# Optimization experiments

Hardware: AMD Instinct MI355X
Metric: run time of the kernel (lower is better)

The kernel has to match this reference:

```python
import jax, jax.numpy as jnp
import numpy as np

NUM_USERS = 100000
NUM_ITEMS = 50000
N_NODES = NUM_USERS + NUM_ITEMS
D = 64                 # embed_dim (= user/item/cate embed dims)
NNZ = 2400000          # sparse adjacency nnz (avg degree 16)
B = 4096               # batch size
HIST = 50              # item history length (max)
UHIST = 30             # user history length (max)
MC = 5                 # max categories per item
NC = 1000              # num_cates
CONCAT = 3 * D         # 192 = user/item concat dim
INNER = 2 * CONCAT     # 384 = MLP expansion factor 2
NUM_GNN_LAYERS = 3


def setup_inputs() -> dict:
    ks = jax.random.split(jax.random.key(0), 20)
    emb_table = jax.random.normal(ks[0], (N_NODES, D), jnp.float32) * 0.02
    cate_table = jax.random.normal(ks[1], (NC, D), jnp.float32) * 0.02
    adj_rows = jax.random.randint(ks[2], (NNZ,), 0, N_NODES, jnp.int32)
    adj_cols = jax.random.randint(ks[3], (NNZ,), 0, N_NODES, jnp.int32)
    adj_vals = jax.random.uniform(ks[4], (NNZ,), jnp.float32) * (1.0 / 16.0)
    cates = jax.random.randint(ks[5], (NUM_ITEMS, MC), 0, NC, jnp.int32)
    cate_lens = jax.random.randint(ks[6], (NUM_ITEMS,), 1, MC + 1, jnp.int32)
    users = jax.random.randint(ks[7], (B,), 0, NUM_USERS, jnp.int32)
    items = jax.random.randint(ks[8], (B,), 0, NUM_ITEMS, jnp.int32)
    item_history_matrix = jax.random.randint(ks[9], (B, HIST), 0, NUM_ITEMS, jnp.int32)
    item_history_len = jax.random.randint(ks[10], (B,), 1, HIST + 1, jnp.int32)
    user_history_matrix = jax.random.randint(ks[11], (B, UHIST), 0, NUM_USERS, jnp.int32)
    user_history_len = jax.random.randint(ks[12], (B,), 1, UHIST + 1, jnp.int32)
    # 4 PreNormResidual MLP blocks: [user_mlp, user_mlp_2, item_mlp, item_mlp_2]
    mlp_ln_w = jnp.ones((4, CONCAT), jnp.float32)
    mlp_ln_b = jnp.zeros((4, CONCAT), jnp.float32)
    mlp_w1 = jax.random.normal(ks[13], (4, CONCAT, INNER), jnp.float32) * 0.05
    mlp_b1 = jnp.zeros((4, INNER), jnp.float32)
    mlp_w2 = jax.random.normal(ks[14], (4, INNER, CONCAT), jnp.float32) * 0.05
    mlp_b2 = jnp.zeros((4, CONCAT), jnp.float32)
    return dict(emb_table=emb_table, cate_table=cate_table, adj_vals=adj_vals,
                mlp_ln_w=mlp_ln_w, mlp_ln_b=mlp_ln_b, mlp_w1=mlp_w1, mlp_b1=mlp_b1,
                mlp_w2=mlp_w2, mlp_b2=mlp_b2, adj_rows=adj_rows, adj_cols=adj_cols,
                cates=cates, cate_lens=cate_lens, users=users, items=items,
                item_history_matrix=item_history_matrix, item_history_len=item_history_len,
                user_history_matrix=user_history_matrix, user_history_len=user_history_len)


def _avg_pool(emb, lens):
    # emb: [..., L, D], lens: [...] -> masked mean over L (matches average_pooling)
    L = emb.shape[-2]
    mask = (jnp.arange(L) < lens[..., None]).astype(emb.dtype)[..., None]
    s = jnp.sum(emb * mask, axis=-2)
    c = jnp.sum(mask, axis=-2) + 1e-9
    return s / c


def _layernorm(x, w, b, eps=1e-5):
    mu = jnp.mean(x, axis=-1, keepdims=True)
    var = jnp.mean(jnp.square(x - mu), axis=-1, keepdims=True)
    return (x - mu) * jax.lax.rsqrt(var + eps) * w + b


def _forward(emb_table, cate_table, adj_vals, mlp_ln_w, mlp_ln_b, mlp_w1, mlp_b1,
             mlp_w2, mlp_b2, adj_rows, adj_cols, cates, cate_lens, users, items,
             item_history_matrix, item_history_len, user_history_matrix, user_history_len):
    n = emb_table.shape[0]
    # GNN propagation: mean of [e0, e1, e2, e3], e_{k+1} = A @ e_k (SpMM via segment_sum)
    e = emb_table
    acc = emb_table
    for _ in range(NUM_GNN_LAYERS):
        msgs = adj_vals[:, None] * e[adj_cols]          # [nnz, D]
        e = jax.ops.segment_sum(msgs, adj_rows, num_segments=n)
        acc = acc + e
    gnn = acc / float(NUM_GNN_LAYERS + 1)
    # --- user features ---
    static_u = gnn[users]                               # [B, D]
    hist_item = emb_table[item_history_matrix + NUM_USERS]   # [B, H, D]
    hc = cates[item_history_matrix]                     # [B, H, MC]
    hcl = cate_lens[item_history_matrix]                # [B, H]
    hce = cate_table[hc]                                # [B, H, MC, D]
    avg_cate = _avg_pool(hce, hcl)                      # [B, H, D]
    hist_with_cate = jnp.concatenate([hist_item, avg_cate], axis=-1)  # [B, H, 2D]
    user_hist = _avg_pool(hist_with_cate, item_history_len)           # [B, 2D]
    uf = jnp.concatenate([static_u, user_hist], axis=-1)              # [B, 3D]
    # --- item features ---
    static_i = gnn[items + NUM_USERS]                   # [B, D]
    ice = cate_table[cates[items]]                      # [B, MC, D]
    avg_ic = _avg_pool(ice, cate_lens[items])           # [B, D]
    item_with_cate = jnp.concatenate([static_i, avg_ic], axis=-1)     # [B, 2D]
    hu = emb_table[user_history_matrix]                 # [B, Hu, D]
    item_hist = _avg_pool(hu, user_history_len)         # [B, D]
    itf = jnp.concatenate([item_with_cate, item_hist], axis=-1)       # [B, 3D]
    # --- PreNormResidual MLP blocks ---
    def block(x, i):
        y = _layernorm(x, mlp_ln_w[i], mlp_ln_b[i])
        h = jax.nn.relu(y @ mlp_w1[i] + mlp_b1[i])
        return h @ mlp_w2[i] + mlp_b2[i] + x
    ue = block(uf, 0) + block(uf, 1)
    ie = block(itf, 2) + block(itf, 3)
    ue = ue / jnp.maximum(jnp.linalg.norm(ue, axis=-1, keepdims=True), 1e-12)
    ie = ie / jnp.maximum(jnp.linalg.norm(ie, axis=-1, keepdims=True), 1e-12)
    return ue, ie


def reference(emb_table, cate_table, adj_vals, mlp_ln_w, mlp_ln_b, mlp_w1, mlp_b1,
              mlp_w2, mlp_b2, adj_rows, adj_cols, cates, cate_lens, users, items,
              item_history_matrix, item_history_len, user_history_matrix, user_history_len):
    return _forward(emb_table, cate_table, adj_vals, mlp_ln_w, mlp_ln_b, mlp_w1, mlp_b1,
                    mlp_w2, mlp_b2, adj_rows, adj_cols, cates, cate_lens, users, items,
                    item_history_matrix, item_history_len, user_history_matrix, user_history_len)
```

## Files before the change

kernel.cpp:

```cpp
#include <hip/hip_runtime.h>
#include <hip/hip_bf16.h>
#include <cstdint>
#include <cstddef>

#define NU      100000
#define NN      150000
#define DDIM    64
#define NNZ_C   2400000
#define B_C     4096
#define HIST_C  50
#define UHIST_C 30
#define MC_C    5
#define CDIM    192
#define IDIM    384

#define NBUK    1176
#define BCAP    2560
#define SCAP    44
#define EPB     8192
#define EDGEH   293
#define FEAT_BLKS 2048
#define CONV_BLKS2 144
#define EMBC_BLKS 1172
#define SPMM_BLKS 4704
#define MARK_BLKS 1408

#define OFF_E1BF   0
#define OFF_E2BF   4816896
#define OFF_EMBBF  9633792
#define OFF_BKT    14433792
#define OFF_GCNT   20454912
#define OFF_SFB    20456192
#define OFF_FLAG   20460928
#define OFF_SDEG   20611456
#define OFF_SEDG   20619648
#define OFF_SIDX   21340544
#define OFF_ROWOFF 21491072
#define OFF_RDEG   21641600
#define OFF_UF     21792128
#define OFF_ITF    22578560
#define OFF_W1T    23364992
#define OFF_W2T    23512448
#define OFF_YBF    14433792
#define OFF_HBF    16006656
#define OFF_ZU     0
#define OFF_ZI     786432

typedef __bf16 bf16x8 __attribute__((ext_vector_type(8)));
typedef __bf16 bf16x4 __attribute__((ext_vector_type(4)));
typedef float f32x4 __attribute__((ext_vector_type(4)));

__device__ inline float4 ldb(const __bf16* p) {
  bf16x4 v = *(const bf16x4*)p;
  return make_float4((float)v[0], (float)v[1], (float)v[2], (float)v[3]);
}
__device__ inline void stb(__bf16* p, float4 o) {
  bf16x4 v;
  v[0] = (__bf16)o.x; v[1] = (__bf16)o.y; v[2] = (__bf16)o.z; v[3] = (__bf16)o.w;
  *(bf16x4*)p = v;
}

__device__ inline void xr4(float4& a) {
  a.x += __shfl_xor(a.x, 16, 64); a.y += __shfl_xor(a.y, 16, 64);
  a.z += __shfl_xor(a.z, 16, 64); a.w += __shfl_xor(a.w, 16, 64);
  a.x += __shfl_xor(a.x, 32, 64); a.y += __shfl_xor(a.y, 32, 64);
  a.z += __shfl_xor(a.z, 32, 64); a.w += __shfl_xor(a.w, 32, 64);
}

__global__ __launch_bounds__(256) void seedflag_kernel(
    const int* __restrict__ users, const int* __restrict__ items,
    int* __restrict__ sfb, int* __restrict__ sidx, int* __restrict__ flag) {
  int t = blockIdx.x * 256 + threadIdx.x;
  if (t >= 2 * B_C) return;
  int s = (t < B_C) ? users[t] : items[t - B_C] + NU;
  atomicOr(&sfb[s >> 5], (int)(1u << (s & 31)));
  sidx[s] = t;
  flag[s] = 1;
}

__global__ __launch_bounds__(256) void mega_kernel(
    const int* __restrict__ rows, const int* __restrict__ cols,
    const float* __restrict__ vals, const int* __restrict__ sfb,
    const int* __restrict__ sidx, int* __restrict__ sdeg,
    int2* __restrict__ sedg, int* __restrict__ gcnt, int2* __restrict__ bkt,
    const float* __restrict__ emb, const float* __restrict__ cate_table,
    const int* __restrict__ cates, const int* __restrict__ cate_lens,
    const int* __restrict__ items, const int* __restrict__ ihm,
    const int* __restrict__ ihl, const int* __restrict__ uhm,
    const int* __restrict__ uhl, float* __restrict__ uf,
    float* __restrict__ itf,
    const float* __restrict__ w1, const float* __restrict__ w2,
    __bf16* __restrict__ w1t, __bf16* __restrict__ w2t,
    __bf16* __restrict__ embbf) {
  __shared__ float tlds[64 * 65];
  __shared__ int hist[NBUK];
  __shared__ int cur[NBUK];
  int blk = blockIdx.x;
  if (blk < EDGEH) {
    int t = threadIdx.x;
    for (int i = t; i < NBUK; i += 256) hist[i] = 0;
    __syncthreads();
    int base = blk * EPB;
    for (int k = 0; k < EPB / 256; ++k) {
      int e = base + k * 256 + t;
      if (e < NNZ_C) atomicAdd(&hist[rows[e] >> 7], 1);
    }
    __syncthreads();
    for (int i = t; i < NBUK; i += 256) {
      int h = hist[i];
      cur[i] = h ? atomicAdd(&gcnt[i], h) : 0;
    }
    __syncthreads();
    for (int k = 0; k < EPB / 256; ++k) {
      int e = base + k * 256 + t;
      if (e < NNZ_C) {
        int r = rows[e], c = cols[e];
        float v = vals[e];
        int bk2 = r >> 7;
        int slot = atomicAdd(&cur[bk2], 1);
        if (slot < BCAP)
          bkt[(size_t)bk2 * BCAP + slot] = make_int2(((r & 127) << 18) | c, __float_as_int(v));
        if ((sfb[r >> 5] >> (r & 31)) & 1) {
          int si = sidx[r];
          int p = atomicAdd(&sdeg[si], 1);
          if (p < SCAP) sedg[(size_t)si * SCAP + p] = make_int2(c, __float_as_int(v));
        }
      }
    }
  } else if (blk < EDGEH + FEAT_BLKS) {
    int tid = threadIdx.x;
    int wave = tid >> 6, w = tid & 63, g = w >> 4, li = w & 15;
    int q = (blk - EDGEH) * 4 + wave;
    if (q < B_C) {
      int b = q;
      int len = ihl[b];
      float4 su = {0.f, 0.f, 0.f, 0.f}, sc = {0.f, 0.f, 0.f, 0.f};
      for (int h = g; h < len; h += 4) {
        int it = ihm[b * HIST_C + h];
        const float4 iv = *(const float4*)(emb + ((size_t)NU + it) * DDIM + li * 4);
        su.x += iv.x; su.y += iv.y; su.z += iv.z; su.w += iv.w;
        int cl = cate_lens[it];
        int id[5];
#pragma unroll
        for (int c = 0; c < 5; ++c) id[c] = cates[it * MC_C + c];
        float4 cs = {0.f, 0.f, 0.f, 0.f};
#pragma unroll
        for (int c = 0; c < 5; ++c) {
          if (c < cl) {
            const float4 cv = *(const float4*)(cate_table + (size_t)id[c] * DDIM + li * 4);
            cs.x += cv.x; cs.y += cv.y; cs.z += cv.z; cs.w += cv.w;
          }
        }
        float icl = 1.f / (float)cl;
        sc.x += cs.x * icl; sc.y += cs.y * icl; sc.z += cs.z * icl; sc.w += cs.w * icl;
      }
      xr4(su); xr4(sc);
      float inv = 1.f / (float)len;
      float* urow = uf + (size_t)b * CDIM;
      if (g == 0) {
        float4 o = {su.x * inv, su.y * inv, su.z * inv, su.w * inv};
        *(float4*)(urow + 64 + li * 4) = o;
      } else if (g == 1) {
        float4 o = {sc.x * inv, sc.y * inv, sc.z * inv, sc.w * inv};
        *(float4*)(urow + 128 + li * 4) = o;
      }
    } else {
      int b = q - B_C;
      int it = items[b];
      int cl = cate_lens[it];
      float4 cs = {0.f, 0.f, 0.f, 0.f};
      for (int c = g; c < cl; c += 4) {
        const float4 cv = *(const float4*)(cate_table + (size_t)cates[it * MC_C + c] * DDIM + li * 4);
        cs.x += cv.x; cs.y += cv.y; cs.z += cv.z; cs.w += cv.w;
      }
      int ul = uhl[b];
      float4 hs = {0.f, 0.f, 0.f, 0.f};
      for (int h = g; h < ul; h += 4) {
        const float4 hv = *(const float4*)(emb + (size_t)uhm[b * UHIST_C + h] * DDIM + li * 4);
        hs.x += hv.x; hs.y += hv.y; hs.z += hv.z; hs.w += hv.w;
      }
      xr4(cs); xr4(hs);
      float* irow = itf + (size_t)b * CDIM;
      if (g == 0) {
        float icl = 1.f / (float)cl;
        float4 o = {cs.x * icl, cs.y * icl, cs.z * icl, cs.w * icl};
        *(float4*)(irow + 64 + li * 4) = o;
      } else if (g == 1) {
        float iul = 1.f / (float)ul;
        float4 o = {hs.x * iul, hs.y * iul, hs.z * iul, hs.w * iul};
        *(float4*)(irow + 128 + li * 4) = o;
      }
    }
  } else if (blk < EDGEH + FEAT_BLKS + CONV_BLKS2) {
    int tile = blk - EDGEH - FEAT_BLKS;
    int t = threadIdx.x;
    if (tile < 72) {
      int p = tile / 18, r = tile % 18, kt = r / 6, nt = r % 6;
      int k0 = kt * 64, n0 = nt * 64;
      const float* srcp = w1 + (size_t)p * (CDIM * IDIM);
#pragma unroll
      for (int i = 0; i < 16; ++i) {
        int idx = i * 256 + t;
        int kl = idx >> 6, nl = idx & 63;
        tlds[kl * 65 + nl] = srcp[(size_t)(k0 + kl) * IDIM + n0 + nl];
      }
      __syncthreads();
#pragma unroll
      for (int i = 0; i < 16; ++i) {
        int idx = i * 256 + t;
        int nl = idx >> 6, kl = idx & 63;
        w1t[((size_t)p * IDIM + n0 + nl) * CDIM + k0 + kl] = (__bf16)tlds[kl * 65 + nl];
      }
    } else {
      int t2 = tile - 72;
      int p = t2 / 18, r = t2 % 18, kt = r / 3, nt = r % 3;
      int k0 = kt * 64, n0 = nt * 64;
      const float* srcp = w2 + (size_t)p * (IDIM * CDIM);
#pragma unroll
      for (int i = 0; i < 16; ++i) {
        int idx = i * 256 + t;
        int kl = idx >> 6, nl = idx & 63;
        tlds[kl * 65 + nl] = srcp[(size_t)(k0 + kl) * CDIM + n0 + nl];
      }
      __syncthreads();
#pragma unroll
      for (int i = 0; i < 16; ++i) {
        int idx = i * 256 + t;
        int nl = idx >> 6, kl = idx & 63;
        w2t[((size_t)p * CDIM + n0 + nl) * IDIM + k0 + kl] = (__bf16)tlds[kl * 65 + nl];
      }
    }
  } else {
    int base = (blk - EDGEH - FEAT_BLKS - CONV_BLKS2) * 2048 + threadIdx.x;
#pragma unroll
    for (int k = 0; k < 8; ++k) {
      int gidx = base + k * 256;
      if (gidx < 2400000) {
        float4 v = ((const float4*)emb)[gidx];
        stb(embbf + (size_t)gidx * 4, v);
      }
    }
  }
}

__global__ __launch_bounds__(256) void bucket_sort(
    int2* bkt, const int* __restrict__ gcnt,
    int* __restrict__ rowoff, int* __restrict__ rdeg,
    const int* __restrict__ sdeg, const int2* __restrict__ sedg,
    int* __restrict__ flag) {
  __shared__ int hcnt[128];
  __shared__ int pre[130];
  __shared__ int cur[128];
  int bk = blockIdx.x, t = threadIdx.x;
  if (bk >= NBUK) {
    int t2 = (bk - NBUK) * 256 + t;
    int si = t2 / SCAP, j = t2 - si * SCAP;
    if (si < 2 * B_C) {
      int n = sdeg[si]; if (n > SCAP) n = SCAP;
      if (j < n) flag[sedg[(size_t)si * SCAP + j].x] = 1;
    }
    return;
  }
  int n = gcnt[bk]; if (n > BCAP) n = BCAP;
  size_t base = (size_t)bk * BCAP;
  if (t < 128) hcnt[t] = 0;
  __syncthreads();
  int ecol[10], eval[10], erow[10];
#pragma unroll
  for (int k = 0; k < 10; ++k) {
    int i = k * 256 + t;
    erow[k] = -1;
    if (i < n) {
      int2 e = bkt[base + i];
      int r = (unsigned)e.x >> 18;
      ecol[k] = e.x & 0x3FFFF;
      eval[k] = e.y;
      erow[k] = r;
      atomicAdd(&hcnt[r], 1);
    }
  }
  __syncthreads();
  if (t == 0) pre[0] = 0;
  if (t < 128) pre[t + 1] = hcnt[t];
  __syncthreads();
  for (int off = 1; off <= 128; off <<= 1) {
    int v = 0;
    if (t <= 128 && t >= off) v = pre[t - off];
    __syncthreads();
    if (t <= 128 && t >= off) pre[t] += v;
    __syncthreads();
  }
  if (t < 128) cur[t] = pre[t];
  __syncthreads();
#pragma unroll
  for (int k = 0; k < 10; ++k) {
    if (erow[k] >= 0) {
      int slot = atomicAdd(&cur[erow[k]], 1);
      bkt[base + slot] = make_int2(ecol[k], eval[k]);
    }
  }
  if (t < 128) {
    rowoff[bk * 128 + t] = (int)base + pre[t];
    rdeg[bk * 128 + t] = hcnt[t];
  }
}

template<int PRED>
__global__ __launch_bounds__(256) void spmm_csr(
    const __bf16* __restrict__ src, __bf16* __restrict__ dst,
    const int* __restrict__ rowoff, const int* __restrict__ rdeg,
    const int2* __restrict__ bkt, const int* __restrict__ flag) {
  int t = threadIdx.x;
  int wave = t >> 6, w = t & 63, g = w >> 4, li = w & 15;
  int la4 = li * 4;
  int row0 = blockIdx.x * 32 + (wave * 4 + g) * 2;
#pragma unroll
  for (int rr = 0; rr < 2; ++rr) {
    int row = row0 + rr;
    if (PRED && flag[row] == 0) continue;
    int off = rowoff[row];
    int n = rdeg[row];
    const int2* ep = bkt + off;
    float4 a0 = {0.f, 0.f, 0.f, 0.f}, a1 = {0.f, 0.f, 0.f, 0.f};
    float4 a2 = {0.f, 0.f, 0.f, 0.f}, a3 = {0.f, 0.f, 0.f, 0.f};
    int j = 0;
    for (; j + 8 <= n; j += 8) {
      int2 e0 = ep[j], e1 = ep[j + 1], e2 = ep[j + 2], e3 = ep[j + 3];
      int2 e4 = ep[j + 4], e5 = ep[j + 5], e6 = ep[j + 6], e7 = ep[j + 7];
      const float4 s0 = ldb(src + (size_t)e0.x * DDIM + la4);
      const float4 s1 = ldb(src + (size_t)e1.x * DDIM + la4);
      const float4 s2 = ldb(src + (size_t)e2.x * DDIM + la4);
      const float4 s3 = ldb(src + (size_t)e3.x * DDIM + la4);
      const float4 s4 = ldb(src + (size_t)e4.x * DDIM + la4);
      const float4 s5 = ldb(src + (size_t)e5.x * DDIM + la4);
      const float4 s6 = ldb(src + (size_t)e6.x * DDIM + la4);
      const float4 s7 = ldb(src + (size_t)e7.x * DDIM + la4);
      float v0 = __int_as_float(e0.y), v1 = __int_as_float(e1.y);
      float v2 = __int_as_float(e2.y), v3 = __int_as_float(e3.y);
      float v4 = __int_as_float(e4.y), v5 = __int_as_float(e5.y);
      float v6 = __int_as_float(e6.y), v7 = __int_as_float(e7.y);
      a0.x += v0 * s0.x; a0.y += v0 * s0.y; a0.z += v0 * s0.z; a0.w += v0 * s0.w;
      a1.x += v1 * s1.x; a1.y += v1 * s1.y; a1.z += v1 * s1.z; a1.w += v1 * s1.w;
      a2.x += v2 * s2.x; a2.y += v2 * s2.y; a2.z += v2 * s2.z; a2.w += v2 * s2.w;
      a3.x += v3 * s3.x; a3.y += v3 * s3.y; a3.z += v3 * s3.z; a3.w += v3 * s3.w;
      a0.x += v4 * s4.x; a0.y += v4 * s4.y; a0.z += v4 * s4.z; a0.w += v4 * s4.w;
      a1.x += v5 * s5.x; a1.y += v5 * s5.y; a1.z += v5 * s5.z; a1.w += v5 * s5.w;
      a2.x += v6 * s6.x; a2.y += v6 * s6.y; a2.z += v6 * s6.z; a2.w += v6 * s6.w;
      a3.x += v7 * s7.x; a3.y += v7 * s7.y; a3.z += v7 * s7.z; a3.w += v7 * s7.w;
    }
    for (; j + 2 <= n; j += 2) {
      int2 e0 = ep[j], e1 = ep[j + 1];
      const float4 s0 = ldb(src + (size_t)e0.x * DDIM + la4);
      const float4 s1 = ldb(src + (size_t)e1.x * DDIM + la4);
      float v0 = __int_as_float(e0.y), v1 = __int_as_float(e1.y);
      a0.x += v0 * s0.x; a0.y += v0 * s0.y; a0.z += v0 * s0.z; a0.w += v0 * s0.w;
      a1.x += v1 * s1.x; a1.y += v1 * s1.y; a1.z += v1 * s1.z; a1.w += v1 * s1.w;
    }
    if (j < n) {
      int2 e0 = ep[j];
      const float4 s0 = ldb(src + (size_t)e0.x * DDIM + la4);
      float v0 = __int_as_float(e0.y);
      a0.x += v0 * s0.x; a0.y += v0 * s0.y; a0.z += v0 * s0.z; a0.w += v0 * s0.w;
    }
    float4 o = {a0.x + a1.x + a2.x + a3.x, a0.y + a1.y + a2.y + a3.y,
                a0.z + a1.z + a2.z + a3.z, a0.w + a1.w + a2.w + a3.w};
    stb(dst + (size_t)row * DDIM + la4, o);
  }
}

__global__ __launch_bounds__(256) void seed_finish(
    const float* __restrict__ emb, const __bf16* __restrict__ e1bf,
    const __bf16* __restrict__ e2bf, const int* __restrict__ sidx,
    const int* __restrict__ sdeg, const int2* __restrict__ sedg,
    const int* __restrict__ users, const int* __restrict__ items,
    float* __restrict__ uf, float* __restrict__ itf) {
  int tid = threadIdx.x;
  int wave = tid >> 6, w = tid & 63, g = w >> 4, li = w & 15;
  int qi = blockIdx.x * 16 + wave * 4 + g;
  int s = (qi < B_C) ? users[qi] : items[qi - B_C] + NU;
  int si = sidx[s];
  int n = sdeg[si]; if (n > SCAP) n = SCAP;
  const int2* ep = sedg + (size_t)si * SCAP;
  float4 a0 = {0.f, 0.f, 0.f, 0.f}, a1 = {0.f, 0.f, 0.f, 0.f};
  float4 a2 = {0.f, 0.f, 0.f, 0.f}, a3 = {0.f, 0.f, 0.f, 0.f};
  int j = 0;
  for (; j + 4 <= n; j += 4) {
    int2 e0 = ep[j], e1v = ep[j + 1], e2v = ep[j + 2], e3v = ep[j + 3];
    const float4 s0 = ldb(e2bf + (size_t)e0.x * DDIM + li * 4);
    const float4 s1 = ldb(e2bf + (size_t)e1v.x * DDIM + li * 4);
    const float4 s2 = ldb(e2bf + (size_t)e2v.x * DDIM + li * 4);
    const float4 s3 = ldb(e2bf + (size_t)e3v.x * DDIM + li * 4);
    float v0 = __int_as_float(e0.y), v1 = __int_as_float(e1v.y);
    float v2 = __int_as_float(e2v.y), v3 = __int_as_float(e3v.y);
    a0.x += v0 * s0.x; a0.y += v0 * s0.y; a0.z += v0 * s0.z; a0.w += v0 * s0.w;
    a1.x += v1 * s1.x; a1.y += v1 * s1.y; a1.z += v1 * s1.z; a1.w += v1 * s1.w;
    a2.x += v2 * s2.x; a2.y += v2 * s2.y; a2.z += v2 * s2.z; a2.w += v2 * s2.w;
    a3.x += v3 * s3.x; a3.y += v3 * s3.y; a3.z += v3 * s3.z; a3.w += v3 * s3.w;
  }
  for (; j < n; ++j) {
    int2 e0 = ep[j];
    const float4 s0 = ldb(e2bf + (size_t)e0.x * DDIM + li * 4);
    float v0 = __int_as_float(e0.y);
    a0.x += v0 * s0.x; a0.y += v0 * s0.y; a0.z += v0 * s0.z; a0.w += v0 * s0.w;
  }
  const float4 e0v = *(const float4*)(emb + (size_t)s * DDIM + li * 4);
  const float4 e1r = ldb(e1bf + (size_t)s * DDIM + li * 4);
  const float4 e2r = ldb(e2bf + (size_t)s * DDIM + li * 4);
  float4 o;
  o.x = (e0v.x + e1r.x + e2r.x + a0.x + a1.x + a2.x + a3.x) * 0.25f;
  o.y = (e0v.y + e1r.y + e2r.y + a0.y + a1.y + a2.y + a3.y) * 0.25f;
  o.z = (e0v.z + e1r.z + e2r.z + a0.z + a1.z + a2.z + a3.z) * 0.25f;
  o.w = (e0v.w + e1r.w + e2r.w + a0.w + a1.w + a2.w + a3.w) * 0.25f;
  float* row = (qi < B_C) ? uf + (size_t)qi * CDIM : itf + (size_t)(qi - B_C) * CDIM;
  *(float4*)(row + li * 4) = o;
}

__global__ __launch_bounds__(64) void ln_kernel(
    const float* __restrict__ uf, const float* __restrict__ itf,
    const float* __restrict__ lnw, const float* __restrict__ lnb,
    __bf16* __restrict__ ybf) {
  int b = blockIdx.x, p = blockIdx.y, t = threadIdx.x;
  const float* x = ((p < 2) ? uf : itf) + (size_t)b * CDIM;
  float v0 = x[t], v1 = x[t + 64], v2 = x[t + 128];
  float s = v0 + v1 + v2;
#pragma unroll
  for (int off = 32; off; off >>= 1) s += __shfl_down(s, off, 64);
  float mu = __shfl(s, 0, 64) * (1.f / 192.f);
  float d0 = v0 - mu, d1 = v1 - mu, d2 = v2 - mu;
  float q = d0 * d0 + d1 * d1 + d2 * d2;
#pragma unroll
  for (int off = 32; off; off >>= 1) q += __shfl_down(q, off, 64);
  float var = __shfl(q, 0, 64) * (1.f / 192.f);
  float rs = 1.f / sqrtf(var + 1e-5f);
  __bf16* yo = ybf + ((size_t)p * B_C + b) * CDIM;
  const float* w = lnw + p * CDIM;
  const float* bb = lnb + p * CDIM;
  yo[t]       = (__bf16)(d0 * rs * w[t]       + bb[t]);
  yo[t + 64]  = (__bf16)(d1 * rs * w[t + 64]  + bb[t + 64]);
  yo[t + 128] = (__bf16)(d2 * rs * w[t + 128] + bb[t + 128]);
}

__global__ __launch_bounds__(256) void gemm1_mfma(
    const __bf16* __restrict__ ybf, const __bf16* __restrict__ w1t,
    const float* __restrict__ b1, __bf16* __restrict__ hbf) {
  int p = blockIdx.z;
  const __bf16* A = ybf + (size_t)p * B_C * CDIM;
  const __bf16* Bt = w1t + (size_t)p * IDIM * CDIM;
  int wave = threadIdx.x >> 6, lane = threadIdx.x & 63;
  int q = lane >> 4, n16 = lane & 15;
  int r0 = blockIdx.x * 64 + wave * 16;
  int c0 = blockIdx.y * 64;
  f32x4 acc[4] = {{0.f, 0.f, 0.f, 0.f}, {0.f, 0.f, 0.f, 0.f},
                  {0.f, 0.f, 0.f, 0.f}, {0.f, 0.f, 0.f, 0.f}};
#pragma unroll
  for (int k0 = 0; k0 < CDIM; k0 += 32) {
    bf16x8 a = *(const bf16x8*)(A + (size_t)(r0 + n16) * CDIM + k0 + q * 8);
#pragma unroll
    for (int c = 0; c < 4; ++c) {
      bf16x8 b = *(const bf16x8*)(Bt + (size_t)(c0 + c * 16 + n16) * CDIM + k0 + q * 8);
      acc[c] = __builtin_amdgcn_mfma_f32_16x16x32_bf16(a, b, acc[c], 0, 0, 0);
    }
  }
#pragma unroll
  for (int c = 0; c < 4; ++c) {
    int col = c0 + c * 16 + n16;
    float bias = b1[p * IDIM + col];
#pragma unroll
    for (int r = 0; r < 4; ++r) {
      int row = r0 + q * 4 + r;
      float v = fmaxf(acc[c][r] + bias, 0.f);
      hbf[((size_t)p * B_C + row) * IDIM + col] = (__bf16)v;
    }
  }
}

__global__ __launch_bounds__(256) void gemm2_mfma(
    const __bf16* __restrict__ hbf, const __bf16* __restrict__ w2t,
    const float* __restrict__ b2, const float* __restrict__ uf,
    const float* __restrict__ itf, float* __restrict__ zu, float* __restrict__ zi) {
  int s = blockIdx.z;
  const float* X = s ? itf : uf;
  float* Z = s ? zi : zu;
  int wave = threadIdx.x >> 6, lane = threadIdx.x & 63;
  int q = lane >> 4, n16 = lane & 15;
  int r0 = blockIdx.x * 64 + wave * 16;
  int c0 = blockIdx.y * 64;
  f32x4 acc[4] = {{0.f, 0.f, 0.f, 0.f}, {0.f, 0.f, 0.f, 0.f},
                  {0.f, 0.f, 0.f, 0.f}, {0.f, 0.f, 0.f, 0.f}};
#pragma unroll
  for (int pi = 0; pi < 2; ++pi) {
    int p = s * 2 + pi;
    const __bf16* A = hbf + (size_t)p * B_C * IDIM;
    const __bf16* Bt = w2t + (size_t)p * CDIM * IDIM;
#pragma unroll
    for (int k0 = 0; k0 < IDIM; k0 += 32) {
      bf16x8 a = *(const bf16x8*)(A + (size_t)(r0 + n16) * IDIM + k0 + q * 8);
#pragma unroll
      for (int c = 0; c < 4; ++c) {
        bf16x8 b = *(const bf16x8*)(Bt + (size_t)(c0 + c * 16 + n16) * IDIM + k0 + q * 8);
        acc[c] = __builtin_amdgcn_mfma_f32_16x16x32_bf16(a, b, acc[c], 0, 0, 0);
      }
    }
  }
#pragma unroll
  for (int c = 0; c < 4; ++c) {
    int col = c0 + c * 16 + n16;
    float bs = b2[(s * 2) * CDIM + col] + b2[(s * 2 + 1) * CDIM + col];
#pragma unroll
    for (int r = 0; r < 4; ++r) {
      int row = r0 + q * 4 + r;
      float xv = X[(size_t)row * CDIM + col];
      Z[(size_t)row * CDIM + col] = acc[c][r] + bs + 2.f * xv;
    }
  }
}

__global__ __launch_bounds__(64) void norm_kernel(
    const float* __restrict__ zu, const float* __restrict__ zi,
    float* __restrict__ out) {
  int b = blockIdx.x, s = blockIdx.y, t = threadIdx.x;
  const float* z = (s ? zi : zu) + (size_t)b * CDIM;
  float v0 = z[t], v1 = z[t + 64], v2 = z[t + 128];
  float q = v0 * v0 + v1 * v1 + v2 * v2;
#pragma unroll
  for (int off = 32; off; off >>= 1) q += __shfl_down(q, off, 64);
  float n = sqrtf(__shfl(q, 0, 64));
  float inv = 1.f / fmaxf(n, 1e-12f);
  float* o = out + (size_t)s * B_C * CDIM + (size_t)b * CDIM;
  o[t] = v0 * inv;
  o[t + 64] = v1 * inv;
  o[t + 128] = v2 * inv;
}

extern "C" void kernel_launch(void* const* d_in, const int* in_sizes, int n_in,
                              void* d_out, int out_size, void* d_ws, size_t ws_size,
                              hipStream_t stream) {
  const float* emb   = (const float*)d_in[0];
  const float* cate  = (const float*)d_in[1];
  const float* avals = (const float*)d_in[2];
  const float* lnw   = (const float*)d_in[3];
  const float* lnb   = (const float*)d_in[4];
  const float* w1    = (const float*)d_in[5];
  const float* b1    = (const float*)d_in[6];
  const float* w2    = (const float*)d_in[7];
  const float* b2    = (const float*)d_in[8];
  const int* arows   = (const int*)d_in[9];
  const int* acols   = (const int*)d_in[10];
  const int* cates_  = (const int*)d_in[11];
  const int* clens   = (const int*)d_in[12];
  const int* users   = (const int*)d_in[13];
  const int* items   = (const int*)d_in[14];
  const int* ihm     = (const int*)d_in[15];
  const int* ihl     = (const int*)d_in[16];
  const int* uhm     = (const int*)d_in[17];
  const int* uhl     = (const int*)d_in[18];
  float* out = (float*)d_out;

  float* W = (float*)d_ws;
  __bf16* e1bf  = (__bf16*)(W + OFF_E1BF);
  __bf16* e2bf  = (__bf16*)(W + OFF_E2BF);
  __bf16* embbf = (__bf16*)(W + OFF_EMBBF);
  int2*   bkt   = (int2*)(W + OFF_BKT);
  int*    gcnt  = (int*)(W + OFF_GCNT);
  int*    sfb   = (int*)(W + OFF_SFB);
  int*    flag  = (int*)(W + OFF_FLAG);
  int*    sdeg  = (int*)(W + OFF_SDEG);
  int2*   sedg  = (int2*)(W + OFF_SEDG);
  int*    sidx  = (int*)(W + OFF_SIDX);
  int*    rowoff= (int*)(W + OFF_ROWOFF);
  int*    rdeg  = (int*)(W + OFF_RDEG);
  float*  uf    = W + OFF_UF;
  float*  itf   = W + OFF_ITF;
  __bf16* w1t   = (__bf16*)(W + OFF_W1T);
  __bf16* w2t   = (__bf16*)(W + OFF_W2T);
  __bf16* ybf   = (__bf16*)(W + OFF_YBF);
  __bf16* hbf   = (__bf16*)(W + OFF_HBF);
  float*  zu    = W + OFF_ZU;
  float*  zi    = W + OFF_ZI;

  (void)hipMemsetAsync(gcnt, 0, (size_t)(OFF_SEDG - OFF_GCNT) * sizeof(int), stream);

  seedflag_kernel<<<(2 * B_C + 255) / 256, 256, 0, stream>>>(users, items, sfb, sidx, flag);

  mega_kernel<<<EDGEH + FEAT_BLKS + CONV_BLKS2 + EMBC_BLKS, 256, 0, stream>>>(
      arows, acols, avals, sfb, sidx, sdeg, sedg, gcnt, bkt,
      emb, cate, cates_, clens, items, ihm, ihl, uhm, uhl, uf, itf,
      w1, w2, w1t, w2t, embbf);

  bucket_sort<<<NBUK + MARK_BLKS, 256, 0, stream>>>(bkt, gcnt, rowoff, rdeg,
                                                    sdeg, sedg, flag);

  spmm_csr<0><<<SPMM_BLKS, 256, 0, stream>>>(embbf, e1bf, rowoff, rdeg, bkt, flag);
  spmm_csr<1><<<SPMM_BLKS, 256, 0, stream>>>(e1bf, e2bf, rowoff, rdeg, bkt, flag);

  seed_finish<<<(2 * B_C) / 16, 256, 0, stream>>>(emb, e1bf, e2bf, sidx, sdeg,
                                                  sedg, users, items, uf, itf);

  ln_kernel<<<dim3(B_C, 4), 64, 0, stream>>>(uf, itf, lnw, lnb, ybf);
  gemm1_mfma<<<dim3(B_C / 64, IDIM / 64, 4), 256, 0, stream>>>(ybf, w1t, b1, hbf);
  gemm2_mfma<<<dim3(B_C / 64, CDIM / 64, 2), 256, 0, stream>>>(hbf, w2t, b2, uf, itf, zu, zi);
  norm_kernel<<<dim3(B_C, 2), 64, 0, stream>>>(zu, zi, out);
}
```

Baseline: 448.5 us.

## Split edge bucketing into histogram, per-bucket prefix scan, and scatter kernels

Replaces the single-pass bucketing, which used global atomics on per-bucket counters, with three passes. The mega kernel now writes per-block bucket histograms to memory, a new prefix kernel scans them per bucket to get deterministic write offsets, and a separate scatter kernel places the edges. This removes global atomic contention and lets the edge blocks be smaller (4096 edges per block), at the cost of two extra kernel launches, an extra read of the row array, and a count/offset matrix of about 0.7M entries each. The memset now starts at sfb instead of gcnt, because gcnt is written directly by the prefix kernel.

```diff
diff --git a/kernel.cpp b/kernel.cpp
--- a/kernel.cpp
+++ b/kernel.cpp
@@ -17,8 +17,8 @@
 #define NBUK    1176
 #define BCAP    2560
 #define SCAP    44
-#define EPB     8192
-#define EDGEH   293
+#define EPB     4096
+#define EDGEP   586
 #define FEAT_BLKS 2048
 #define CONV_BLKS2 144
 #define EMBC_BLKS 1172
@@ -41,6 +41,8 @@
 #define OFF_ITF    22578560
 #define OFF_W1T    23364992
 #define OFF_W2T    23512448
+#define OFF_CNT    23659904
+#define OFF_OFFA   24349040
 #define OFF_YBF    14433792
 #define OFF_HBF    16006656
 #define OFF_ZU     0
@@ -79,10 +81,7 @@
 }
 
 __global__ __launch_bounds__(256) void mega_kernel(
-    const int* __restrict__ rows, const int* __restrict__ cols,
-    const float* __restrict__ vals, const int* __restrict__ sfb,
-    const int* __restrict__ sidx, int* __restrict__ sdeg,
-    int2* __restrict__ sedg, int* __restrict__ gcnt, int2* __restrict__ bkt,
+    const int* __restrict__ rows, int* __restrict__ cnt,
     const float* __restrict__ emb, const float* __restrict__ cate_table,
     const int* __restrict__ cates, const int* __restrict__ cate_lens,
     const int* __restrict__ items, const int* __restrict__ ihm,
@@ -94,43 +93,23 @@
     __bf16* __restrict__ embbf) {
   __shared__ float tlds[64 * 65];
   __shared__ int hist[NBUK];
-  __shared__ int cur[NBUK];
   int blk = blockIdx.x;
-  if (blk < EDGEH) {
+  if (blk < EDGEP) {
     int t = threadIdx.x;
     for (int i = t; i < NBUK; i += 256) hist[i] = 0;
     __syncthreads();
     int base = blk * EPB;
+#pragma unroll
     for (int k = 0; k < EPB / 256; ++k) {
       int e = base + k * 256 + t;
       if (e < NNZ_C) atomicAdd(&hist[rows[e] >> 7], 1);
     }
     __syncthreads();
-    for (int i = t; i < NBUK; i += 256) {
-      int h = hist[i];
-      cur[i] = h ? atomicAdd(&gcnt[i], h) : 0;
-    }
-    __syncthreads();
-    for (int k = 0; k < EPB / 256; ++k) {
-      int e = base + k * 256 + t;
-      if (e < NNZ_C) {
-        int r = rows[e], c = cols[e];
-        float v = vals[e];
-        int bk2 = r >> 7;
-        int slot = atomicAdd(&cur[bk2], 1);
-        if (slot < BCAP)
-          bkt[(size_t)bk2 * BCAP + slot] = make_int2(((r & 127) << 18) | c, __float_as_int(v));
-        if ((sfb[r >> 5] >> (r & 31)) & 1) {
-          int si = sidx[r];
-          int p = atomicAdd(&sdeg[si], 1);
-          if (p < SCAP) sedg[(size_t)si * SCAP + p] = make_int2(c, __float_as_int(v));
-        }
-      }
-    }
-  } else if (blk < EDGEH + FEAT_BLKS) {
+    for (int i = t; i < NBUK; i += 256) cnt[(size_t)blk * NBUK + i] = hist[i];
+  } else if (blk < EDGEP + FEAT_BLKS) {
     int tid = threadIdx.x;
     int wave = tid >> 6, w = tid & 63, g = w >> 4, li = w & 15;
-    int q = (blk - EDGEH) * 4 + wave;
+    int q = (blk - EDGEP) * 4 + wave;
     if (q < B_C) {
       int b = q;
       int len = ihl[b];
@@ -191,8 +170,8 @@
         *(float4*)(irow + 128 + li * 4) = o;
       }
     }
-  } else if (blk < EDGEH + FEAT_BLKS + CONV_BLKS2) {
-    int tile = blk - EDGEH - FEAT_BLKS;
+  } else if (blk < EDGEP + FEAT_BLKS + CONV_BLKS2) {
+    int tile = blk - EDGEP - FEAT_BLKS;
     int t = threadIdx.x;
     if (tile < 72) {
       int p = tile / 18, r = tile % 18, kt = r / 6, nt = r % 6;
@@ -231,13 +210,70 @@
       }
     }
   } else {
-    int base = (blk - EDGEH - FEAT_BLKS - CONV_BLKS2) * 2048 + threadIdx.x;
+    int base = (blk - EDGEP - FEAT_BLKS - CONV_BLKS2) * 2048 + threadIdx.x;
 #pragma unroll
     for (int k = 0; k < 8; ++k) {
       int gidx = base + k * 256;
       if (gidx < 2400000) {
         float4 v = ((const float4*)emb)[gidx];
         stb(embbf + (size_t)gidx * 4, v);
+      }
+    }
+  }
+}
+
+__global__ __launch_bounds__(256) void prefix_kernel(
+    const int* __restrict__ cnt, int* __restrict__ offa, int* __restrict__ gcnt) {
+  __shared__ int s[EDGEP];
+  int bk = blockIdx.x, t = threadIdx.x;
+  for (int i = t; i < EDGEP; i += 256) s[i] = cnt[(size_t)i * NBUK + bk];
+  __syncthreads();
+  for (int off = 1; off < EDGEP; off <<= 1) {
+    int i0 = t, i1 = t + 256, i2 = t + 512;
+    int v0 = 0, v1 = 0, v2 = 0;
+    if (i0 < EDGEP && i0 >= off) v0 = s[i0 - off];
+    if (i1 < EDGEP && i1 >= off) v1 = s[i1 - off];
+    if (i2 < EDGEP && i2 >= off) v2 = s[i2 - off];
+    __syncthreads();
+    if (i0 < EDGEP && i0 >= off) s[i0] += v0;
+    if (i1 < EDGEP && i1 >= off) s[i1] += v1;
+    if (i2 < EDGEP && i2 >= off) s[i2] += v2;
+    __syncthreads();
+  }
+  int basebk = bk * BCAP;
+  for (int i = t; i < EDGEP; i += 256) {
+    int incl = s[i];
+    int c = cnt[(size_t)i * NBUK + bk];
+    offa[(size_t)i * NBUK + bk] = basebk + incl - c;
+  }
+  if (t == 0) gcnt[bk] = s[EDGEP - 1];
+}
+
+__global__ __launch_bounds__(256) void scatter_kernel(
+    const int* __restrict__ rows, const int* __restrict__ cols,
+    const float* __restrict__ vals, const int* __restrict__ offa,
+    int2* __restrict__ bkt, const int* __restrict__ sfb,
+    const int* __restrict__ sidx, int* __restrict__ sdeg,
+    int2* __restrict__ sedg) {
+  __shared__ int cur[NBUK];
+  int blk = blockIdx.x, t = threadIdx.x;
+  for (int i = t; i < NBUK; i += 256) cur[i] = offa[(size_t)blk * NBUK + i];
+  __syncthreads();
+  int base = blk * EPB;
+#pragma unroll
+  for (int k = 0; k < EPB / 256; ++k) {
+    int e = base + k * 256 + t;
+    if (e < NNZ_C) {
+      int r = rows[e], c = cols[e];
+      int vi = __float_as_int(vals[e]);
+      int bk2 = r >> 7;
+      int slot = atomicAdd(&cur[bk2], 1);
+      if (slot - bk2 * BCAP < BCAP)
+        bkt[slot] = make_int2(((r & 127) << 18) | c, vi);
+      if ((sfb[r >> 5] >> (r & 31)) & 1) {
+        int si = sidx[r];
+        int p = atomicAdd(&sdeg[si], 1);
+        if (p < SCAP) sedg[(size_t)si * SCAP + p] = make_int2(c, vi);
       }
     }
   }
@@ -573,19 +609,26 @@
   float*  itf   = W + OFF_ITF;
   __bf16* w1t   = (__bf16*)(W + OFF_W1T);
   __bf16* w2t   = (__bf16*)(W + OFF_W2T);
+  int*    cnt   = (int*)(W + OFF_CNT);
+  int*    offa  = (int*)(W + OFF_OFFA);
   __bf16* ybf   = (__bf16*)(W + OFF_YBF);
   __bf16* hbf   = (__bf16*)(W + OFF_HBF);
   float*  zu    = W + OFF_ZU;
   float*  zi    = W + OFF_ZI;
 
-  (void)hipMemsetAsync(gcnt, 0, (size_t)(OFF_SEDG - OFF_GCNT) * sizeof(int), stream);
+  (void)hipMemsetAsync(sfb, 0, (size_t)(OFF_SEDG - OFF_SFB) * sizeof(int), stream);
 
   seedflag_kernel<<<(2 * B_C + 255) / 256, 256, 0, stream>>>(users, items, sfb, sidx, flag);
 
-  mega_kernel<<<EDGEH + FEAT_BLKS + CONV_BLKS2 + EMBC_BLKS, 256, 0, stream>>>(
-      arows, acols, avals, sfb, sidx, sdeg, sedg, gcnt, bkt,
+  mega_kernel<<<EDGEP + FEAT_BLKS + CONV_BLKS2 + EMBC_BLKS, 256, 0, stream>>>(
+      arows, cnt,
       emb, cate, cates_, clens, items, ihm, ihl, uhm, uhl, uf, itf,
       w1, w2, w1t, w2t, embbf);
+
+  prefix_kernel<<<NBUK, 256, 0, stream>>>(cnt, offa, gcnt);
+
+  scatter_kernel<<<EDGEP, 256, 0, stream>>>(arows, acols, avals, offa, bkt,
+                                            sfb, sidx, sdeg, sedg);
 
   bucket_sort<<<NBUK + MARK_BLKS, 256, 0, stream>>>(bkt, gcnt, rowoff, rdeg,
                                                     sdeg, sedg, flag);
```

New measurement: 451.0 us. Within noise of the previous version (+0.6%).
